# Optimization experiments

Measured on AMD Instinct MI355X. Metric: run time of the kernel, lower is better.

Reference implementation:

```python
import jax, jax.numpy as jnp
import numpy as np

B, T, I = 8192, 20, 16
H1, H2, FC = 128, 64, 32


def _lstm(x_tbi, Wih, Whh, bih, bhh, H):
    """PyTorch-convention LSTM. x_tbi: (T,B,in). Gate order: i,f,g,o. Returns (T,B,H) hidden seq."""
    Tn, Bn = x_tbi.shape[0], x_tbi.shape[1]
    # precompute input projection for all timesteps: (T,B,4H)
    xz = jnp.einsum('tbi,gi->tbg', x_tbi, Wih) + (bih + bhh)

    def step(carry, xz_t):
        h, c = carry
        z = xz_t + h @ Whh.T  # (B,4H)
        i = jax.nn.sigmoid(z[:, 0*H:1*H])
        f = jax.nn.sigmoid(z[:, 1*H:2*H])
        g = jnp.tanh(z[:, 2*H:3*H])
        o = jax.nn.sigmoid(z[:, 3*H:4*H])
        c = f * c + i * g
        h = o * jnp.tanh(c)
        return (h, c), h

    h0 = jnp.zeros((Bn, H), x_tbi.dtype)
    c0 = jnp.zeros((Bn, H), x_tbi.dtype)
    _, hs = jax.lax.scan(step, (h0, c0), xz)
    return hs  # (T,B,H)


def setup_inputs() -> dict:
    key = jax.random.key(0)
    ks = jax.random.split(key, 16)
    s1 = 1.0 / np.sqrt(H1)
    s2 = 1.0 / np.sqrt(H2)
    u = lambda k, shape, s: jax.random.uniform(k, shape, jnp.float32, -s, s)
    return {
        'x': jax.random.normal(ks[0], (B, T, I), jnp.float32),
        'Wih1': u(ks[1], (4 * H1, I), s1),
        'Whh1': u(ks[2], (4 * H1, H1), s1),
        'bih1': u(ks[3], (4 * H1,), s1),
        'bhh1': u(ks[4], (4 * H1,), s1),
        'Wih2': u(ks[5], (4 * H2, H1), s2),
        'Whh2': u(ks[6], (4 * H2, H2), s2),
        'bih2': u(ks[7], (4 * H2,), s2),
        'bhh2': u(ks[8], (4 * H2,), s2),
        'gamma': jnp.ones((H2,), jnp.float32),
        'beta': jnp.zeros((H2,), jnp.float32),
        'W1': u(ks[9], (FC, H2), 1.0 / np.sqrt(H2)),
        'b1': u(ks[10], (FC,), 1.0 / np.sqrt(H2)),
        'W2': u(ks[11], (1, FC), 1.0 / np.sqrt(FC)),
        'b2': u(ks[12], (1,), 1.0 / np.sqrt(FC)),
    }


def reference(x, Wih1, Whh1, bih1, bhh1, Wih2, Whh2, bih2, bhh2, gamma, beta, W1, b1, W2, b2):
    # dropout layers are identity (eval mode)
    x_tbi = jnp.transpose(x, (1, 0, 2))           # (T,B,I)
    out1 = _lstm(x_tbi, Wih1, Whh1, bih1, bhh1, H1)  # (T,B,H1)
    out2 = _lstm(out1, Wih2, Whh2, bih2, bhh2, H2)   # (T,B,H2)
    last = out2[-1]                               # (B,H2)
    # LayerNorm over H2
    mu = jnp.mean(last, axis=-1, keepdims=True)
    var = jnp.mean((last - mu) ** 2, axis=-1, keepdims=True)
    normed = (last - mu) * jax.lax.rsqrt(var + 1e-5) * gamma + beta
    h = jax.nn.relu(normed @ W1.T + b1)           # (B,FC)
    logit = h @ W2.T + b2                         # (B,1)
    return logit[:, 0]
```

## Files before the change

kernel.cpp:

```cpp
#include <hip/hip_runtime.h>

#define TS 20
#define BATCH 8192
#define LOG2E 1.4426950408889634f

typedef _Float16 half8 __attribute__((ext_vector_type(8)));
typedef float f32x4 __attribute__((ext_vector_type(4)));

__device__ __forceinline__ float fexp2(float x) {
#if __has_builtin(__builtin_amdgcn_exp2f)
    return __builtin_amdgcn_exp2f(x);
#else
    return exp2f(x);
#endif
}
__device__ __forceinline__ float sig2(float zp)  { return __builtin_amdgcn_rcpf(1.0f + fexp2(-zp)); }
__device__ __forceinline__ float tanh2(float zp) { return 1.0f - 2.0f * __builtin_amdgcn_rcpf(1.0f + fexp2(zp)); }
__device__ __forceinline__ int swz(int r) { return (r & 7) ^ (((r >> 3) & 1) << 2); }

extern "C" __global__ __launch_bounds__(512, 1)
void fused_lstm_kernel(const float* __restrict__ x,
                       const float* __restrict__ Wih1, const float* __restrict__ Whh1,
                       const float* __restrict__ bih1, const float* __restrict__ bhh1,
                       const float* __restrict__ Wih2, const float* __restrict__ Whh2,
                       const float* __restrict__ bih2, const float* __restrict__ bhh2,
                       const float* __restrict__ gamma, const float* __restrict__ beta,
                       const float* __restrict__ W1fc, const float* __restrict__ b1fc,
                       const float* __restrict__ W2fc, const float* __restrict__ b2fc,
                       float* __restrict__ out)
{
    __shared__ __align__(16) _Float16 bf2l[4 * 4 * 6 * 64 * 8];
    __shared__ __align__(16) _Float16 Hb[2][2][16][128];
    __shared__ __align__(16) _Float16 Hc[2][2][16][72];
    __shared__ __align__(16) _Float16 Xb[32][328];
    __shared__ float h2f[32][68];

    const int tid  = threadIdx.x;
    const int lane = tid & 63;
    const int w    = tid >> 6;
    const int lrow = lane & 15;
    const int lgrp = lane >> 4;
    const int b0   = blockIdx.x * 32;

    half8 bf[4][5];
    float bias1[4];
#pragma unroll
    for (int g = 0; g < 4; ++g) {
        const float sc = (g == 2) ? 2.0f * LOG2E : LOG2E;
        const int n = g * 128 + w * 16 + lrow;
        bias1[g] = (bih1[n] + bhh1[n]) * sc;
#pragma unroll
        for (int ch = 0; ch < 5; ++ch) {
            half8 v;
            if (ch < 4) {
                const float4 p0 = *(const float4*)&Whh1[n * 128 + ch * 32 + lgrp * 8];
                const float4 p1 = *(const float4*)&Whh1[n * 128 + ch * 32 + lgrp * 8 + 4];
                v[0]=(_Float16)(p0.x*sc); v[1]=(_Float16)(p0.y*sc); v[2]=(_Float16)(p0.z*sc); v[3]=(_Float16)(p0.w*sc);
                v[4]=(_Float16)(p1.x*sc); v[5]=(_Float16)(p1.y*sc); v[6]=(_Float16)(p1.z*sc); v[7]=(_Float16)(p1.w*sc);
            } else if (lgrp < 2) {
                const float4 p0 = *(const float4*)&Wih1[n * 16 + lgrp * 8];
                const float4 p1 = *(const float4*)&Wih1[n * 16 + lgrp * 8 + 4];
                v[0]=(_Float16)(p0.x*sc); v[1]=(_Float16)(p0.y*sc); v[2]=(_Float16)(p0.z*sc); v[3]=(_Float16)(p0.w*sc);
                v[4]=(_Float16)(p1.x*sc); v[5]=(_Float16)(p1.y*sc); v[6]=(_Float16)(p1.z*sc); v[7]=(_Float16)(p1.w*sc);
            } else {
#pragma unroll
                for (int j = 0; j < 8; ++j) v[j] = (_Float16)0.0f;
            }
            bf[g][ch] = v;
        }
    }

    const int cg = w & 3;
    const int mt = w >> 2;
    float bias2[4];
#pragma unroll
    for (int g = 0; g < 4; ++g) {
        const float sc = (g == 2) ? 2.0f * LOG2E : LOG2E;
        const int n = g * 64 + cg * 16 + lrow;
        bias2[g] = (bih2[n] + bhh2[n]) * sc;
    }
    if (w < 4) {
#pragma unroll
        for (int g = 0; g < 4; ++g) {
            const float sc = (g == 2) ? 2.0f * LOG2E : LOG2E;
            const int n = g * 64 + w * 16 + lrow;
#pragma unroll
            for (int ch = 0; ch < 6; ++ch) {
                const float4 p0 = (ch < 4) ? *(const float4*)&Wih2[n * 128 + ch * 32 + lgrp * 8]
                                           : *(const float4*)&Whh2[n * 64 + (ch - 4) * 32 + lgrp * 8];
                const float4 p1 = (ch < 4) ? *(const float4*)&Wih2[n * 128 + ch * 32 + lgrp * 8 + 4]
                                           : *(const float4*)&Whh2[n * 64 + (ch - 4) * 32 + lgrp * 8 + 4];
                half8 v;
                v[0]=(_Float16)(p0.x*sc); v[1]=(_Float16)(p0.y*sc); v[2]=(_Float16)(p0.z*sc); v[3]=(_Float16)(p0.w*sc);
                v[4]=(_Float16)(p1.x*sc); v[5]=(_Float16)(p1.y*sc); v[6]=(_Float16)(p1.z*sc); v[7]=(_Float16)(p1.w*sc);
                ((half8*)bf2l)[((w * 4 + g) * 6 + ch) * 64 + lane] = v;
            }
        }
    }

    for (int i = tid; i < 2 * 2 * 16 * 128; i += 512) (&Hb[0][0][0][0])[i] = (_Float16)0.0f;
    for (int i = tid; i < 2 * 2 * 16 * 72;  i += 512) (&Hc[0][0][0][0])[i] = (_Float16)0.0f;
    for (int i = tid; i < 32 * 320; i += 512) {
        const int r = i / 320, k = i % 320;
        Xb[r][k] = (_Float16)x[(size_t)(b0 + r) * 320 + k];
    }
    half8 kzero;
#pragma unroll
    for (int j = 0; j < 8; ++j) kzero[j] = (_Float16)0.0f;

    float c1[2][4] = {{0.f,0.f,0.f,0.f},{0.f,0.f,0.f,0.f}};
    float c2[4] = {0.f, 0.f, 0.f, 0.f};
    const int hu  = (w << 1) | (lrow >> 3);
    const int hlo = lrow & 7;
    const int szr = swz(lrow);
    const int cell2 = (cg << 4) | lrow;

    __syncthreads();

    for (int t = 0; t < TS; ++t) {
        const int s = t & 1;
        f32x4 z[2][4];
#pragma unroll
        for (int tile = 0; tile < 2; ++tile)
#pragma unroll
            for (int g = 0; g < 4; ++g) z[tile][g] = (f32x4){bias1[g], bias1[g], bias1[g], bias1[g]};
#pragma unroll
        for (int ch = 0; ch < 5; ++ch) {
#pragma unroll
            for (int tile = 0; tile < 2; ++tile) {
                half8 a;
                if (ch < 4) a = *(const half8*)&Hb[s ^ 1][tile][lrow][(((ch << 2) | lgrp) ^ szr) * 8];
                else        a = (lgrp < 2) ? *(const half8*)&Xb[tile * 16 + lrow][t * 16 + lgrp * 8] : kzero;
#pragma unroll
                for (int g = 0; g < 4; ++g)
                    z[tile][g] = __builtin_amdgcn_mfma_f32_16x16x32_f16(a, bf[g][ch], z[tile][g], 0, 0, 0);
            }
        }
#pragma unroll
        for (int tile = 0; tile < 2; ++tile)
#pragma unroll
            for (int j = 0; j < 4; ++j) {
                const float iv = sig2 (z[tile][0][j]);
                const float fv = sig2 (z[tile][1][j]);
                const float gv = tanh2(z[tile][2][j]);
                const float ov = sig2 (z[tile][3][j]);
                const float cn = fv * c1[tile][j] + iv * gv;
                c1[tile][j] = cn;
                const float h = ov * tanh2(2.0f * LOG2E * cn);
                const int m = (lgrp << 2) | j;
                Hb[s][tile][m][((hu ^ swz(m)) << 3) | hlo] = (_Float16)h;
            }
        __syncthreads();
        {
            half8 a2[6];
#pragma unroll
            for (int ch = 0; ch < 4; ++ch)
                a2[ch] = *(const half8*)&Hb[s][mt][lrow][(((ch << 2) | lgrp) ^ szr) * 8];
#pragma unroll
            for (int ch = 4; ch < 6; ++ch)
                a2[ch] = *(const half8*)&Hc[s ^ 1][mt][lrow][(ch - 4) * 32 + lgrp * 8];
            f32x4 z2[4];
#pragma unroll
            for (int g = 0; g < 4; ++g) {
                f32x4 acc = {bias2[g], bias2[g], bias2[g], bias2[g]};
#pragma unroll
                for (int ch = 0; ch < 6; ++ch) {
                    const half8 bfrag = ((const half8*)bf2l)[((cg * 4 + g) * 6 + ch) * 64 + lane];
                    acc = __builtin_amdgcn_mfma_f32_16x16x32_f16(a2[ch], bfrag, acc, 0, 0, 0);
                }
                z2[g] = acc;
            }
#pragma unroll
            for (int j = 0; j < 4; ++j) {
                const float iv = sig2 (z2[0][j]);
                const float fv = sig2 (z2[1][j]);
                const float gv = tanh2(z2[2][j]);
                const float ov = sig2 (z2[3][j]);
                const float cn = fv * c2[j] + iv * gv;
                c2[j] = cn;
                const float h = ov * tanh2(2.0f * LOG2E * cn);
                const int m = (lgrp << 2) | j;
                Hc[s][mt][m][cell2] = (_Float16)h;
                if (t == TS - 1) h2f[(mt << 4) | m][cell2] = h;
            }
        }
    }
    __syncthreads();

    {
        const int m = tid >> 4, q = tid & 15;
        const float v0 = h2f[m][q * 4 + 0];
        const float v1 = h2f[m][q * 4 + 1];
        const float v2 = h2f[m][q * 4 + 2];
        const float v3 = h2f[m][q * 4 + 3];
        float ssum = v0 + v1 + v2 + v3;
        ssum += __shfl_xor(ssum, 1); ssum += __shfl_xor(ssum, 2);
        ssum += __shfl_xor(ssum, 4); ssum += __shfl_xor(ssum, 8);
        const float mean = ssum * (1.0f / 64.0f);
        const float d0 = v0 - mean, d1 = v1 - mean, d2 = v2 - mean, d3 = v3 - mean;
        float vs = d0 * d0 + d1 * d1 + d2 * d2 + d3 * d3;
        vs += __shfl_xor(vs, 1); vs += __shfl_xor(vs, 2);
        vs += __shfl_xor(vs, 4); vs += __shfl_xor(vs, 8);
        const float rstd = rsqrtf(vs * (1.0f / 64.0f) + 1e-5f);
        const int i0 = q * 4;
        h2f[m][i0 + 0] = d0 * rstd * gamma[i0 + 0] + beta[i0 + 0];
        h2f[m][i0 + 1] = d1 * rstd * gamma[i0 + 1] + beta[i0 + 1];
        h2f[m][i0 + 2] = d2 * rstd * gamma[i0 + 2] + beta[i0 + 2];
        h2f[m][i0 + 3] = d3 * rstd * gamma[i0 + 3] + beta[i0 + 3];
    }
    __syncthreads();
    {
        const int o = tid & 31;
        const int mgrp = tid >> 5;
#pragma unroll
        for (int rr = 0; rr < 2; ++rr) {
            const int m = mgrp + rr * 16;
            float acc = b1fc[o];
#pragma unroll 8
            for (int k = 0; k < 64; ++k) acc += h2f[m][k] * W1fc[o * 64 + k];
            const float hv = fmaxf(acc, 0.0f);
            float p = hv * W2fc[o];
            p += __shfl_xor(p, 1); p += __shfl_xor(p, 2);
            p += __shfl_xor(p, 4); p += __shfl_xor(p, 8); p += __shfl_xor(p, 16);
            if (o == 0) out[b0 + m] = p + b2fc[0];
        }
    }
}

extern "C" void kernel_launch(void* const* d_in, const int* in_sizes, int n_in,
                              void* d_out, int out_size, void* d_ws, size_t ws_size,
                              hipStream_t stream) {
    (void)in_sizes; (void)n_in; (void)d_ws; (void)ws_size; (void)out_size;
    const float* x_p    = (const float*)d_in[0];
    const float* Wih1_p = (const float*)d_in[1];
    const float* Whh1_p = (const float*)d_in[2];
    const float* bih1_p = (const float*)d_in[3];
    const float* bhh1_p = (const float*)d_in[4];
    const float* Wih2_p = (const float*)d_in[5];
    const float* Whh2_p = (const float*)d_in[6];
    const float* bih2_p = (const float*)d_in[7];
    const float* bhh2_p = (const float*)d_in[8];
    const float* gamma_p = (const float*)d_in[9];
    const float* beta_p  = (const float*)d_in[10];
    const float* W1_p   = (const float*)d_in[11];
    const float* b1_p   = (const float*)d_in[12];
    const float* W2_p   = (const float*)d_in[13];
    const float* b2_p   = (const float*)d_in[14];
    float* out_p = (float*)d_out;

    fused_lstm_kernel<<<dim3(BATCH / 32), dim3(512), 0, stream>>>(
        x_p, Wih1_p, Whh1_p, bih1_p, bhh1_p,
        Wih2_p, Whh2_p, bih2_p, bhh2_p,
        gamma_p, beta_p, W1_p, b1_p, W2_p, b2_p, out_p);
}
```

Before: 77.85 us.

## Split LSTM layers into producer/consumer warp groups with 1024-thread blocks

Doubles the block to 1024 threads: waves 0-7 run layer 1 and waves 8-15 run layer 2 plus the head, so layer 2 at step t overlaps layer 1 at step t+1, coordinated by matched raw s_barrier calls. Layer-2 Wih2 fragments now live in registers and only Whh2 stays in shared memory, cutting LDS reads per step. This relies on an exact match of barrier counts between the two branches and raises register pressure per wave.

```diff
diff --git a/kernel.cpp b/kernel.cpp
--- a/kernel.cpp
+++ b/kernel.cpp
@@ -17,19 +17,23 @@
 __device__ __forceinline__ float sig2(float zp)  { return __builtin_amdgcn_rcpf(1.0f + fexp2(-zp)); }
 __device__ __forceinline__ float tanh2(float zp) { return 1.0f - 2.0f * __builtin_amdgcn_rcpf(1.0f + fexp2(zp)); }
 __device__ __forceinline__ int swz(int r) { return (r & 7) ^ (((r >> 3) & 1) << 2); }
-
-extern "C" __global__ __launch_bounds__(512, 1)
-void fused_lstm_kernel(const float* __restrict__ x,
-                       const float* __restrict__ Wih1, const float* __restrict__ Whh1,
-                       const float* __restrict__ bih1, const float* __restrict__ bhh1,
-                       const float* __restrict__ Wih2, const float* __restrict__ Whh2,
-                       const float* __restrict__ bih2, const float* __restrict__ bhh2,
-                       const float* __restrict__ gamma, const float* __restrict__ beta,
-                       const float* __restrict__ W1fc, const float* __restrict__ b1fc,
-                       const float* __restrict__ W2fc, const float* __restrict__ b2fc,
-                       float* __restrict__ out)
+__device__ __forceinline__ void wg_barrier() {
+    asm volatile("s_waitcnt lgkmcnt(0)" ::: "memory");
+    __builtin_amdgcn_s_barrier();
+}
+
+extern "C" __global__ __launch_bounds__(1024, 4)
+void fused_lstm_pc_kernel(const float* __restrict__ x,
+                          const float* __restrict__ Wih1, const float* __restrict__ Whh1,
+                          const float* __restrict__ bih1, const float* __restrict__ bhh1,
+                          const float* __restrict__ Wih2, const float* __restrict__ Whh2,
+                          const float* __restrict__ bih2, const float* __restrict__ bhh2,
+                          const float* __restrict__ gamma, const float* __restrict__ beta,
+                          const float* __restrict__ W1fc, const float* __restrict__ b1fc,
+                          const float* __restrict__ W2fc, const float* __restrict__ b2fc,
+                          float* __restrict__ out)
 {
-    __shared__ __align__(16) _Float16 bf2l[4 * 4 * 6 * 64 * 8];
+    __shared__ __align__(16) _Float16 bf2l[4 * 4 * 2 * 64 * 8];
     __shared__ __align__(16) _Float16 Hb[2][2][16][128];
     __shared__ __align__(16) _Float16 Hc[2][2][16][72];
     __shared__ __align__(16) _Float16 Xb[32][328];
@@ -42,133 +46,151 @@
     const int lgrp = lane >> 4;
     const int b0   = blockIdx.x * 32;
 
-    half8 bf[4][5];
-    float bias1[4];
-#pragma unroll
-    for (int g = 0; g < 4; ++g) {
-        const float sc = (g == 2) ? 2.0f * LOG2E : LOG2E;
-        const int n = g * 128 + w * 16 + lrow;
-        bias1[g] = (bih1[n] + bhh1[n]) * sc;
-#pragma unroll
-        for (int ch = 0; ch < 5; ++ch) {
-            half8 v;
-            if (ch < 4) {
-                const float4 p0 = *(const float4*)&Whh1[n * 128 + ch * 32 + lgrp * 8];
-                const float4 p1 = *(const float4*)&Whh1[n * 128 + ch * 32 + lgrp * 8 + 4];
-                v[0]=(_Float16)(p0.x*sc); v[1]=(_Float16)(p0.y*sc); v[2]=(_Float16)(p0.z*sc); v[3]=(_Float16)(p0.w*sc);
-                v[4]=(_Float16)(p1.x*sc); v[5]=(_Float16)(p1.y*sc); v[6]=(_Float16)(p1.z*sc); v[7]=(_Float16)(p1.w*sc);
-            } else if (lgrp < 2) {
-                const float4 p0 = *(const float4*)&Wih1[n * 16 + lgrp * 8];
-                const float4 p1 = *(const float4*)&Wih1[n * 16 + lgrp * 8 + 4];
-                v[0]=(_Float16)(p0.x*sc); v[1]=(_Float16)(p0.y*sc); v[2]=(_Float16)(p0.z*sc); v[3]=(_Float16)(p0.w*sc);
-                v[4]=(_Float16)(p1.x*sc); v[5]=(_Float16)(p1.y*sc); v[6]=(_Float16)(p1.z*sc); v[7]=(_Float16)(p1.w*sc);
-            } else {
-#pragma unroll
-                for (int j = 0; j < 8; ++j) v[j] = (_Float16)0.0f;
-            }
-            bf[g][ch] = v;
-        }
+    for (int i = tid; i < 2 * 2 * 16 * 128; i += 1024) (&Hb[0][0][0][0])[i] = (_Float16)0.0f;
+    for (int i = tid; i < 2 * 2 * 16 * 72;  i += 1024) (&Hc[0][0][0][0])[i] = (_Float16)0.0f;
+    for (int i = tid; i < 32 * 320; i += 1024) {
+        const int r = i / 320, k = i % 320;
+        Xb[r][k] = (_Float16)x[(size_t)(b0 + r) * 320 + k];
     }
 
-    const int cg = w & 3;
-    const int mt = w >> 2;
-    float bias2[4];
-#pragma unroll
-    for (int g = 0; g < 4; ++g) {
-        const float sc = (g == 2) ? 2.0f * LOG2E : LOG2E;
-        const int n = g * 64 + cg * 16 + lrow;
-        bias2[g] = (bih2[n] + bhh2[n]) * sc;
-    }
-    if (w < 4) {
+    if (w < 8) {
+        half8 bf[4][5];
+        float bias1[4];
 #pragma unroll
         for (int g = 0; g < 4; ++g) {
             const float sc = (g == 2) ? 2.0f * LOG2E : LOG2E;
-            const int n = g * 64 + w * 16 + lrow;
-#pragma unroll
-            for (int ch = 0; ch < 6; ++ch) {
-                const float4 p0 = (ch < 4) ? *(const float4*)&Wih2[n * 128 + ch * 32 + lgrp * 8]
-                                           : *(const float4*)&Whh2[n * 64 + (ch - 4) * 32 + lgrp * 8];
-                const float4 p1 = (ch < 4) ? *(const float4*)&Wih2[n * 128 + ch * 32 + lgrp * 8 + 4]
-                                           : *(const float4*)&Whh2[n * 64 + (ch - 4) * 32 + lgrp * 8 + 4];
+            const int n = g * 128 + w * 16 + lrow;
+            bias1[g] = (bih1[n] + bhh1[n]) * sc;
+#pragma unroll
+            for (int ch = 0; ch < 5; ++ch) {
+                half8 v;
+                if (ch < 4) {
+                    const float4 p0 = *(const float4*)&Whh1[n * 128 + ch * 32 + lgrp * 8];
+                    const float4 p1 = *(const float4*)&Whh1[n * 128 + ch * 32 + lgrp * 8 + 4];
+                    v[0]=(_Float16)(p0.x*sc); v[1]=(_Float16)(p0.y*sc); v[2]=(_Float16)(p0.z*sc); v[3]=(_Float16)(p0.w*sc);
+                    v[4]=(_Float16)(p1.x*sc); v[5]=(_Float16)(p1.y*sc); v[6]=(_Float16)(p1.z*sc); v[7]=(_Float16)(p1.w*sc);
+                } else if (lgrp < 2) {
+                    const float4 p0 = *(const float4*)&Wih1[n * 16 + lgrp * 8];
+                    const float4 p1 = *(const float4*)&Wih1[n * 16 + lgrp * 8 + 4];
+                    v[0]=(_Float16)(p0.x*sc); v[1]=(_Float16)(p0.y*sc); v[2]=(_Float16)(p0.z*sc); v[3]=(_Float16)(p0.w*sc);
+                    v[4]=(_Float16)(p1.x*sc); v[5]=(_Float16)(p1.y*sc); v[6]=(_Float16)(p1.z*sc); v[7]=(_Float16)(p1.w*sc);
+                } else {
+#pragma unroll
+                    for (int j = 0; j < 8; ++j) v[j] = (_Float16)0.0f;
+                }
+                bf[g][ch] = v;
+            }
+        }
+        half8 kzero;
+#pragma unroll
+        for (int j = 0; j < 8; ++j) kzero[j] = (_Float16)0.0f;
+
+        float c1[2][4] = {{0.f,0.f,0.f,0.f},{0.f,0.f,0.f,0.f}};
+        const int hu  = (w << 1) | (lrow >> 3);
+        const int hlo = lrow & 7;
+        const int szr = swz(lrow);
+
+        wg_barrier();
+        for (int t = 0; t < TS; ++t) {
+            const int s = t & 1;
+            f32x4 z[2][4];
+#pragma unroll
+            for (int tile = 0; tile < 2; ++tile)
+#pragma unroll
+                for (int g = 0; g < 4; ++g) z[tile][g] = (f32x4){bias1[g], bias1[g], bias1[g], bias1[g]};
+#pragma unroll
+            for (int ch = 0; ch < 5; ++ch) {
+#pragma unroll
+                for (int tile = 0; tile < 2; ++tile) {
+                    half8 a;
+                    if (ch < 4) a = *(const half8*)&Hb[s ^ 1][tile][lrow][(((ch << 2) | lgrp) ^ szr) * 8];
+                    else        a = (lgrp < 2) ? *(const half8*)&Xb[tile * 16 + lrow][t * 16 + lgrp * 8] : kzero;
+#pragma unroll
+                    for (int g = 0; g < 4; ++g)
+                        z[tile][g] = __builtin_amdgcn_mfma_f32_16x16x32_f16(a, bf[g][ch], z[tile][g], 0, 0, 0);
+                }
+            }
+#pragma unroll
+            for (int tile = 0; tile < 2; ++tile)
+#pragma unroll
+                for (int j = 0; j < 4; ++j) {
+                    const float iv = sig2 (z[tile][0][j]);
+                    const float fv = sig2 (z[tile][1][j]);
+                    const float gv = tanh2(z[tile][2][j]);
+                    const float ov = sig2 (z[tile][3][j]);
+                    const float cn = fv * c1[tile][j] + iv * gv;
+                    c1[tile][j] = cn;
+                    const float h = ov * tanh2(2.0f * LOG2E * cn);
+                    const int m = (lgrp << 2) | j;
+                    Hb[s][tile][m][((hu ^ swz(m)) << 3) | hlo] = (_Float16)h;
+                }
+            wg_barrier();
+        }
+        wg_barrier();
+        wg_barrier();
+    } else {
+        const int bw = w - 8;
+        const int cg = bw & 3;
+        const int mt = bw >> 2;
+        half8 w2[4][4];
+        float bias2[4];
+#pragma unroll
+        for (int g = 0; g < 4; ++g) {
+            const float sc = (g == 2) ? 2.0f * LOG2E : LOG2E;
+            const int n = g * 64 + cg * 16 + lrow;
+            bias2[g] = (bih2[n] + bhh2[n]) * sc;
+#pragma unroll
+            for (int ch = 0; ch < 4; ++ch) {
+                const float4 p0 = *(const float4*)&Wih2[n * 128 + ch * 32 + lgrp * 8];
+                const float4 p1 = *(const float4*)&Wih2[n * 128 + ch * 32 + lgrp * 8 + 4];
                 half8 v;
                 v[0]=(_Float16)(p0.x*sc); v[1]=(_Float16)(p0.y*sc); v[2]=(_Float16)(p0.z*sc); v[3]=(_Float16)(p0.w*sc);
                 v[4]=(_Float16)(p1.x*sc); v[5]=(_Float16)(p1.y*sc); v[6]=(_Float16)(p1.z*sc); v[7]=(_Float16)(p1.w*sc);
-                ((half8*)bf2l)[((w * 4 + g) * 6 + ch) * 64 + lane] = v;
-            }
-        }
-    }
-
-    for (int i = tid; i < 2 * 2 * 16 * 128; i += 512) (&Hb[0][0][0][0])[i] = (_Float16)0.0f;
-    for (int i = tid; i < 2 * 2 * 16 * 72;  i += 512) (&Hc[0][0][0][0])[i] = (_Float16)0.0f;
-    for (int i = tid; i < 32 * 320; i += 512) {
-        const int r = i / 320, k = i % 320;
-        Xb[r][k] = (_Float16)x[(size_t)(b0 + r) * 320 + k];
-    }
-    half8 kzero;
-#pragma unroll
-    for (int j = 0; j < 8; ++j) kzero[j] = (_Float16)0.0f;
-
-    float c1[2][4] = {{0.f,0.f,0.f,0.f},{0.f,0.f,0.f,0.f}};
-    float c2[4] = {0.f, 0.f, 0.f, 0.f};
-    const int hu  = (w << 1) | (lrow >> 3);
-    const int hlo = lrow & 7;
-    const int szr = swz(lrow);
-    const int cell2 = (cg << 4) | lrow;
-
-    __syncthreads();
-
-    for (int t = 0; t < TS; ++t) {
-        const int s = t & 1;
-        f32x4 z[2][4];
-#pragma unroll
-        for (int tile = 0; tile < 2; ++tile)
-#pragma unroll
-            for (int g = 0; g < 4; ++g) z[tile][g] = (f32x4){bias1[g], bias1[g], bias1[g], bias1[g]};
-#pragma unroll
-        for (int ch = 0; ch < 5; ++ch) {
-#pragma unroll
-            for (int tile = 0; tile < 2; ++tile) {
-                half8 a;
-                if (ch < 4) a = *(const half8*)&Hb[s ^ 1][tile][lrow][(((ch << 2) | lgrp) ^ szr) * 8];
-                else        a = (lgrp < 2) ? *(const half8*)&Xb[tile * 16 + lrow][t * 16 + lgrp * 8] : kzero;
+                w2[g][ch] = v;
+            }
+        }
+        if (bw < 4) {
+#pragma unroll
+            for (int g = 0; g < 4; ++g) {
+                const float sc = (g == 2) ? 2.0f * LOG2E : LOG2E;
+                const int n = g * 64 + bw * 16 + lrow;
+#pragma unroll
+                for (int c2i = 0; c2i < 2; ++c2i) {
+                    const float4 p0 = *(const float4*)&Whh2[n * 64 + c2i * 32 + lgrp * 8];
+                    const float4 p1 = *(const float4*)&Whh2[n * 64 + c2i * 32 + lgrp * 8 + 4];
+                    half8 v;
+                    v[0]=(_Float16)(p0.x*sc); v[1]=(_Float16)(p0.y*sc); v[2]=(_Float16)(p0.z*sc); v[3]=(_Float16)(p0.w*sc);
+                    v[4]=(_Float16)(p1.x*sc); v[5]=(_Float16)(p1.y*sc); v[6]=(_Float16)(p1.z*sc); v[7]=(_Float16)(p1.w*sc);
+                    ((half8*)bf2l)[((bw * 4 + g) * 2 + c2i) * 64 + lane] = v;
+                }
+            }
+        }
+        float c2[4] = {0.f, 0.f, 0.f, 0.f};
+        const int cell2 = (cg << 4) | lrow;
+        const int szr = swz(lrow);
+
+        wg_barrier();
+        for (int t = 0; t < TS; ++t) {
+            const int s = t & 1;
+            wg_barrier();
+            f32x4 z2[4];
+#pragma unroll
+            for (int g = 0; g < 4; ++g) z2[g] = (f32x4){bias2[g], bias2[g], bias2[g], bias2[g]};
+#pragma unroll
+            for (int ch = 0; ch < 4; ++ch) {
+                const half8 a2 = *(const half8*)&Hb[s][mt][lrow][(((ch << 2) | lgrp) ^ szr) * 8];
 #pragma unroll
                 for (int g = 0; g < 4; ++g)
-                    z[tile][g] = __builtin_amdgcn_mfma_f32_16x16x32_f16(a, bf[g][ch], z[tile][g], 0, 0, 0);
-            }
-        }
-#pragma unroll
-        for (int tile = 0; tile < 2; ++tile)
-#pragma unroll
-            for (int j = 0; j < 4; ++j) {
-                const float iv = sig2 (z[tile][0][j]);
-                const float fv = sig2 (z[tile][1][j]);
-                const float gv = tanh2(z[tile][2][j]);
-                const float ov = sig2 (z[tile][3][j]);
-                const float cn = fv * c1[tile][j] + iv * gv;
-                c1[tile][j] = cn;
-                const float h = ov * tanh2(2.0f * LOG2E * cn);
-                const int m = (lgrp << 2) | j;
-                Hb[s][tile][m][((hu ^ swz(m)) << 3) | hlo] = (_Float16)h;
-            }
-        __syncthreads();
-        {
-            half8 a2[6];
-#pragma unroll
-            for (int ch = 0; ch < 4; ++ch)
-                a2[ch] = *(const half8*)&Hb[s][mt][lrow][(((ch << 2) | lgrp) ^ szr) * 8];
-#pragma unroll
-            for (int ch = 4; ch < 6; ++ch)
-                a2[ch] = *(const half8*)&Hc[s ^ 1][mt][lrow][(ch - 4) * 32 + lgrp * 8];
-            f32x4 z2[4];
-#pragma unroll
-            for (int g = 0; g < 4; ++g) {
-                f32x4 acc = {bias2[g], bias2[g], bias2[g], bias2[g]};
-#pragma unroll
-                for (int ch = 0; ch < 6; ++ch) {
-                    const half8 bfrag = ((const half8*)bf2l)[((cg * 4 + g) * 6 + ch) * 64 + lane];
-                    acc = __builtin_amdgcn_mfma_f32_16x16x32_f16(a2[ch], bfrag, acc, 0, 0, 0);
-                }
-                z2[g] = acc;
+                    z2[g] = __builtin_amdgcn_mfma_f32_16x16x32_f16(a2, w2[g][ch], z2[g], 0, 0, 0);
+            }
+#pragma unroll
+            for (int c2i = 0; c2i < 2; ++c2i) {
+                const half8 a2 = *(const half8*)&Hc[s ^ 1][mt][lrow][c2i * 32 + lgrp * 8];
+#pragma unroll
+                for (int g = 0; g < 4; ++g) {
+                    const half8 bfrag = ((const half8*)bf2l)[((cg * 4 + g) * 2 + c2i) * 64 + lane];
+                    z2[g] = __builtin_amdgcn_mfma_f32_16x16x32_f16(a2, bfrag, z2[g], 0, 0, 0);
+                }
             }
 #pragma unroll
             for (int j = 0; j < 4; ++j) {
@@ -184,45 +206,46 @@
                 if (t == TS - 1) h2f[(mt << 4) | m][cell2] = h;
             }
         }
-    }
-    __syncthreads();
-
-    {
-        const int m = tid >> 4, q = tid & 15;
-        const float v0 = h2f[m][q * 4 + 0];
-        const float v1 = h2f[m][q * 4 + 1];
-        const float v2 = h2f[m][q * 4 + 2];
-        const float v3 = h2f[m][q * 4 + 3];
-        float ssum = v0 + v1 + v2 + v3;
-        ssum += __shfl_xor(ssum, 1); ssum += __shfl_xor(ssum, 2);
-        ssum += __shfl_xor(ssum, 4); ssum += __shfl_xor(ssum, 8);
-        const float mean = ssum * (1.0f / 64.0f);
-        const float d0 = v0 - mean, d1 = v1 - mean, d2 = v2 - mean, d3 = v3 - mean;
-        float vs = d0 * d0 + d1 * d1 + d2 * d2 + d3 * d3;
-        vs += __shfl_xor(vs, 1); vs += __shfl_xor(vs, 2);
-        vs += __shfl_xor(vs, 4); vs += __shfl_xor(vs, 8);
-        const float rstd = rsqrtf(vs * (1.0f / 64.0f) + 1e-5f);
-        const int i0 = q * 4;
-        h2f[m][i0 + 0] = d0 * rstd * gamma[i0 + 0] + beta[i0 + 0];
-        h2f[m][i0 + 1] = d1 * rstd * gamma[i0 + 1] + beta[i0 + 1];
-        h2f[m][i0 + 2] = d2 * rstd * gamma[i0 + 2] + beta[i0 + 2];
-        h2f[m][i0 + 3] = d3 * rstd * gamma[i0 + 3] + beta[i0 + 3];
-    }
-    __syncthreads();
-    {
-        const int o = tid & 31;
-        const int mgrp = tid >> 5;
-#pragma unroll
-        for (int rr = 0; rr < 2; ++rr) {
-            const int m = mgrp + rr * 16;
-            float acc = b1fc[o];
+        wg_barrier();
+        {
+            const int bt = tid - 512;
+            const int m = bt >> 4, q = bt & 15;
+            const float v0 = h2f[m][q * 4 + 0];
+            const float v1 = h2f[m][q * 4 + 1];
+            const float v2 = h2f[m][q * 4 + 2];
+            const float v3 = h2f[m][q * 4 + 3];
+            float ssum = v0 + v1 + v2 + v3;
+            ssum += __shfl_xor(ssum, 1); ssum += __shfl_xor(ssum, 2);
+            ssum += __shfl_xor(ssum, 4); ssum += __shfl_xor(ssum, 8);
+            const float mean = ssum * (1.0f / 64.0f);
+            const float d0 = v0 - mean, d1 = v1 - mean, d2 = v2 - mean, d3 = v3 - mean;
+            float vs = d0 * d0 + d1 * d1 + d2 * d2 + d3 * d3;
+            vs += __shfl_xor(vs, 1); vs += __shfl_xor(vs, 2);
+            vs += __shfl_xor(vs, 4); vs += __shfl_xor(vs, 8);
+            const float rstd = rsqrtf(vs * (1.0f / 64.0f) + 1e-5f);
+            const int i0 = q * 4;
+            h2f[m][i0 + 0] = d0 * rstd * gamma[i0 + 0] + beta[i0 + 0];
+            h2f[m][i0 + 1] = d1 * rstd * gamma[i0 + 1] + beta[i0 + 1];
+            h2f[m][i0 + 2] = d2 * rstd * gamma[i0 + 2] + beta[i0 + 2];
+            h2f[m][i0 + 3] = d3 * rstd * gamma[i0 + 3] + beta[i0 + 3];
+        }
+        wg_barrier();
+        {
+            const int bt = tid - 512;
+            const int o = bt & 31;
+            const int mgrp = bt >> 5;
+#pragma unroll
+            for (int rr = 0; rr < 2; ++rr) {
+                const int m = mgrp + rr * 16;
+                float acc = b1fc[o];
 #pragma unroll 8
-            for (int k = 0; k < 64; ++k) acc += h2f[m][k] * W1fc[o * 64 + k];
-            const float hv = fmaxf(acc, 0.0f);
-            float p = hv * W2fc[o];
-            p += __shfl_xor(p, 1); p += __shfl_xor(p, 2);
-            p += __shfl_xor(p, 4); p += __shfl_xor(p, 8); p += __shfl_xor(p, 16);
-            if (o == 0) out[b0 + m] = p + b2fc[0];
+                for (int k = 0; k < 64; ++k) acc += h2f[m][k] * W1fc[o * 64 + k];
+                const float hv = fmaxf(acc, 0.0f);
+                float p = hv * W2fc[o];
+                p += __shfl_xor(p, 1); p += __shfl_xor(p, 2);
+                p += __shfl_xor(p, 4); p += __shfl_xor(p, 8); p += __shfl_xor(p, 16);
+                if (o == 0) out[b0 + m] = p + b2fc[0];
+            }
         }
     }
 }
@@ -248,7 +271,7 @@
     const float* b2_p   = (const float*)d_in[14];
     float* out_p = (float*)d_out;
 
-    fused_lstm_kernel<<<dim3(BATCH / 32), dim3(512), 0, stream>>>(
+    fused_lstm_pc_kernel<<<dim3(BATCH / 32), dim3(1024), 0, stream>>>(
         x_p, Wih1_p, Whh1_p, bih1_p, bhh1_p,
         Wih2_p, Whh2_p, bih2_p, bhh2_p,
         gamma_p, beta_p, W1_p, b1_p, W2_p, b2_p, out_p);
```

New measurement: 127.0 us. 1.63x slower.

## Warp-specialize LSTM layers into pipelined producer and consumer wave groups

Applied to the files above, without the earlier changes.

Waves 0-3 now compute only layer 1 and each covers two gate column groups. Waves 4-7 compute only layer 2, running one timestep behind, so the two layers overlap instead of executing back to back each step. Layer-2 weights move from shared memory into registers, and the per-step barrier becomes a custom one that waits only on LDS traffic before `s_barrier`. The cost is twice the layer-1 MFMA work per producer wave on the critical path, plus higher register pressure.

```diff
diff --git a/kernel.cpp b/kernel.cpp
--- a/kernel.cpp
+++ b/kernel.cpp
@@ -17,19 +17,22 @@
 __device__ __forceinline__ float sig2(float zp)  { return __builtin_amdgcn_rcpf(1.0f + fexp2(-zp)); }
 __device__ __forceinline__ float tanh2(float zp) { return 1.0f - 2.0f * __builtin_amdgcn_rcpf(1.0f + fexp2(zp)); }
 __device__ __forceinline__ int swz(int r) { return (r & 7) ^ (((r >> 3) & 1) << 2); }
+__device__ __forceinline__ void wg_barrier() {
+    asm volatile("s_waitcnt lgkmcnt(0)" ::: "memory");
+    __builtin_amdgcn_s_barrier();
+}
 
 extern "C" __global__ __launch_bounds__(512, 1)
-void fused_lstm_kernel(const float* __restrict__ x,
-                       const float* __restrict__ Wih1, const float* __restrict__ Whh1,
-                       const float* __restrict__ bih1, const float* __restrict__ bhh1,
-                       const float* __restrict__ Wih2, const float* __restrict__ Whh2,
-                       const float* __restrict__ bih2, const float* __restrict__ bhh2,
-                       const float* __restrict__ gamma, const float* __restrict__ beta,
-                       const float* __restrict__ W1fc, const float* __restrict__ b1fc,
-                       const float* __restrict__ W2fc, const float* __restrict__ b2fc,
-                       float* __restrict__ out)
+void fused_lstm_pc8_kernel(const float* __restrict__ x,
+                           const float* __restrict__ Wih1, const float* __restrict__ Whh1,
+                           const float* __restrict__ bih1, const float* __restrict__ bhh1,
+                           const float* __restrict__ Wih2, const float* __restrict__ Whh2,
+                           const float* __restrict__ bih2, const float* __restrict__ bhh2,
+                           const float* __restrict__ gamma, const float* __restrict__ beta,
+                           const float* __restrict__ W1fc, const float* __restrict__ b1fc,
+                           const float* __restrict__ W2fc, const float* __restrict__ b2fc,
+                           float* __restrict__ out)
 {
-    __shared__ __align__(16) _Float16 bf2l[4 * 4 * 6 * 64 * 8];
     __shared__ __align__(16) _Float16 Hb[2][2][16][128];
     __shared__ __align__(16) _Float16 Hc[2][2][16][72];
     __shared__ __align__(16) _Float16 Xb[32][328];
@@ -42,48 +45,107 @@
     const int lgrp = lane >> 4;
     const int b0   = blockIdx.x * 32;
 
-    half8 bf[4][5];
-    float bias1[4];
-#pragma unroll
-    for (int g = 0; g < 4; ++g) {
-        const float sc = (g == 2) ? 2.0f * LOG2E : LOG2E;
-        const int n = g * 128 + w * 16 + lrow;
-        bias1[g] = (bih1[n] + bhh1[n]) * sc;
-#pragma unroll
-        for (int ch = 0; ch < 5; ++ch) {
-            half8 v;
-            if (ch < 4) {
-                const float4 p0 = *(const float4*)&Whh1[n * 128 + ch * 32 + lgrp * 8];
-                const float4 p1 = *(const float4*)&Whh1[n * 128 + ch * 32 + lgrp * 8 + 4];
-                v[0]=(_Float16)(p0.x*sc); v[1]=(_Float16)(p0.y*sc); v[2]=(_Float16)(p0.z*sc); v[3]=(_Float16)(p0.w*sc);
-                v[4]=(_Float16)(p1.x*sc); v[5]=(_Float16)(p1.y*sc); v[6]=(_Float16)(p1.z*sc); v[7]=(_Float16)(p1.w*sc);
-            } else if (lgrp < 2) {
-                const float4 p0 = *(const float4*)&Wih1[n * 16 + lgrp * 8];
-                const float4 p1 = *(const float4*)&Wih1[n * 16 + lgrp * 8 + 4];
-                v[0]=(_Float16)(p0.x*sc); v[1]=(_Float16)(p0.y*sc); v[2]=(_Float16)(p0.z*sc); v[3]=(_Float16)(p0.w*sc);
-                v[4]=(_Float16)(p1.x*sc); v[5]=(_Float16)(p1.y*sc); v[6]=(_Float16)(p1.z*sc); v[7]=(_Float16)(p1.w*sc);
-            } else {
-#pragma unroll
-                for (int j = 0; j < 8; ++j) v[j] = (_Float16)0.0f;
-            }
-            bf[g][ch] = v;
-        }
-    }
-
-    const int cg = w & 3;
-    const int mt = w >> 2;
-    float bias2[4];
-#pragma unroll
-    for (int g = 0; g < 4; ++g) {
-        const float sc = (g == 2) ? 2.0f * LOG2E : LOG2E;
-        const int n = g * 64 + cg * 16 + lrow;
-        bias2[g] = (bih2[n] + bhh2[n]) * sc;
-    }
+    for (int i = tid; i < 2 * 2 * 16 * 128; i += 512) (&Hb[0][0][0][0])[i] = (_Float16)0.0f;
+    for (int i = tid; i < 2 * 2 * 16 * 72;  i += 512) (&Hc[0][0][0][0])[i] = (_Float16)0.0f;
+    for (int i = tid; i < 32 * 320; i += 512) {
+        const int r = i / 320, k = i % 320;
+        Xb[r][k] = (_Float16)x[(size_t)(b0 + r) * 320 + k];
+    }
+
     if (w < 4) {
+        half8 bfw[2][4][5];
+        float bias1[2][4];
+#pragma unroll
+        for (int cgi = 0; cgi < 2; ++cgi) {
+            const int cg = w + cgi * 4;
+#pragma unroll
+            for (int g = 0; g < 4; ++g) {
+                const float sc = (g == 2) ? 2.0f * LOG2E : LOG2E;
+                const int n = g * 128 + cg * 16 + lrow;
+                bias1[cgi][g] = (bih1[n] + bhh1[n]) * sc;
+#pragma unroll
+                for (int ch = 0; ch < 5; ++ch) {
+                    half8 v;
+                    if (ch < 4) {
+                        const float4 p0 = *(const float4*)&Whh1[n * 128 + ch * 32 + lgrp * 8];
+                        const float4 p1 = *(const float4*)&Whh1[n * 128 + ch * 32 + lgrp * 8 + 4];
+                        v[0]=(_Float16)(p0.x*sc); v[1]=(_Float16)(p0.y*sc); v[2]=(_Float16)(p0.z*sc); v[3]=(_Float16)(p0.w*sc);
+                        v[4]=(_Float16)(p1.x*sc); v[5]=(_Float16)(p1.y*sc); v[6]=(_Float16)(p1.z*sc); v[7]=(_Float16)(p1.w*sc);
+                    } else if (lgrp < 2) {
+                        const float4 p0 = *(const float4*)&Wih1[n * 16 + lgrp * 8];
+                        const float4 p1 = *(const float4*)&Wih1[n * 16 + lgrp * 8 + 4];
+                        v[0]=(_Float16)(p0.x*sc); v[1]=(_Float16)(p0.y*sc); v[2]=(_Float16)(p0.z*sc); v[3]=(_Float16)(p0.w*sc);
+                        v[4]=(_Float16)(p1.x*sc); v[5]=(_Float16)(p1.y*sc); v[6]=(_Float16)(p1.z*sc); v[7]=(_Float16)(p1.w*sc);
+                    } else {
+#pragma unroll
+                        for (int j = 0; j < 8; ++j) v[j] = (_Float16)0.0f;
+                    }
+                    bfw[cgi][g][ch] = v;
+                }
+            }
+        }
+        half8 kzero;
+#pragma unroll
+        for (int j = 0; j < 8; ++j) kzero[j] = (_Float16)0.0f;
+
+        float c1[2][2][4] = {{{0.f,0.f,0.f,0.f},{0.f,0.f,0.f,0.f}},
+                             {{0.f,0.f,0.f,0.f},{0.f,0.f,0.f,0.f}}};
+        const int szr = swz(lrow);
+        const int hlo = lrow & 7;
+
+        wg_barrier();
+        for (int t = 0; t < TS; ++t) {
+            const int s = t & 1;
+#pragma unroll
+            for (int tile = 0; tile < 2; ++tile) {
+                half8 a[5];
+#pragma unroll
+                for (int ch = 0; ch < 4; ++ch)
+                    a[ch] = *(const half8*)&Hb[s ^ 1][tile][lrow][(((ch << 2) | lgrp) ^ szr) * 8];
+                a[4] = (lgrp < 2) ? *(const half8*)&Xb[tile * 16 + lrow][t * 16 + lgrp * 8] : kzero;
+
+                f32x4 z[2][4];
+#pragma unroll
+                for (int cgi = 0; cgi < 2; ++cgi)
+#pragma unroll
+                    for (int g = 0; g < 4; ++g)
+                        z[cgi][g] = (f32x4){bias1[cgi][g], bias1[cgi][g], bias1[cgi][g], bias1[cgi][g]};
+#pragma unroll
+                for (int ch = 0; ch < 5; ++ch)
+#pragma unroll
+                    for (int cgi = 0; cgi < 2; ++cgi)
+#pragma unroll
+                        for (int g = 0; g < 4; ++g)
+                            z[cgi][g] = __builtin_amdgcn_mfma_f32_16x16x32_f16(a[ch], bfw[cgi][g][ch], z[cgi][g], 0, 0, 0);
+#pragma unroll
+                for (int cgi = 0; cgi < 2; ++cgi) {
+                    const int cg = w + cgi * 4;
+                    const int hu = (cg << 1) | (lrow >> 3);
+#pragma unroll
+                    for (int j = 0; j < 4; ++j) {
+                        const float iv = sig2 (z[cgi][0][j]);
+                        const float fv = sig2 (z[cgi][1][j]);
+                        const float gv = tanh2(z[cgi][2][j]);
+                        const float ov = sig2 (z[cgi][3][j]);
+                        const float cn = fv * c1[tile][cgi][j] + iv * gv;
+                        c1[tile][cgi][j] = cn;
+                        const float h = ov * tanh2(2.0f * LOG2E * cn);
+                        const int m = (lgrp << 2) | j;
+                        Hb[s][tile][m][((hu ^ swz(m)) << 3) | hlo] = (_Float16)h;
+                    }
+                }
+            }
+            wg_barrier();
+        }
+    } else {
+        const int bw = w - 4;
+        half8 w2[4][6];
+        float bias2[4];
 #pragma unroll
         for (int g = 0; g < 4; ++g) {
             const float sc = (g == 2) ? 2.0f * LOG2E : LOG2E;
-            const int n = g * 64 + w * 16 + lrow;
+            const int n = g * 64 + bw * 16 + lrow;
+            bias2[g] = (bih2[n] + bhh2[n]) * sc;
 #pragma unroll
             for (int ch = 0; ch < 6; ++ch) {
                 const float4 p0 = (ch < 4) ? *(const float4*)&Wih2[n * 128 + ch * 32 + lgrp * 8]
@@ -93,95 +155,48 @@
                 half8 v;
                 v[0]=(_Float16)(p0.x*sc); v[1]=(_Float16)(p0.y*sc); v[2]=(_Float16)(p0.z*sc); v[3]=(_Float16)(p0.w*sc);
                 v[4]=(_Float16)(p1.x*sc); v[5]=(_Float16)(p1.y*sc); v[6]=(_Float16)(p1.z*sc); v[7]=(_Float16)(p1.w*sc);
-                ((half8*)bf2l)[((w * 4 + g) * 6 + ch) * 64 + lane] = v;
-            }
-        }
-    }
-
-    for (int i = tid; i < 2 * 2 * 16 * 128; i += 512) (&Hb[0][0][0][0])[i] = (_Float16)0.0f;
-    for (int i = tid; i < 2 * 2 * 16 * 72;  i += 512) (&Hc[0][0][0][0])[i] = (_Float16)0.0f;
-    for (int i = tid; i < 32 * 320; i += 512) {
-        const int r = i / 320, k = i % 320;
-        Xb[r][k] = (_Float16)x[(size_t)(b0 + r) * 320 + k];
-    }
-    half8 kzero;
-#pragma unroll
-    for (int j = 0; j < 8; ++j) kzero[j] = (_Float16)0.0f;
-
-    float c1[2][4] = {{0.f,0.f,0.f,0.f},{0.f,0.f,0.f,0.f}};
-    float c2[4] = {0.f, 0.f, 0.f, 0.f};
-    const int hu  = (w << 1) | (lrow >> 3);
-    const int hlo = lrow & 7;
-    const int szr = swz(lrow);
-    const int cell2 = (cg << 4) | lrow;
-
-    __syncthreads();
-
-    for (int t = 0; t < TS; ++t) {
-        const int s = t & 1;
-        f32x4 z[2][4];
-#pragma unroll
-        for (int tile = 0; tile < 2; ++tile)
-#pragma unroll
-            for (int g = 0; g < 4; ++g) z[tile][g] = (f32x4){bias1[g], bias1[g], bias1[g], bias1[g]};
-#pragma unroll
-        for (int ch = 0; ch < 5; ++ch) {
+                w2[g][ch] = v;
+            }
+        }
+        float c2[2][4] = {{0.f,0.f,0.f,0.f},{0.f,0.f,0.f,0.f}};
+        const int cell2 = (bw << 4) | lrow;
+        const int szr = swz(lrow);
+
+        wg_barrier();
+        for (int t = 0; t < TS; ++t) {
+            const int s = t & 1;
+            wg_barrier();
 #pragma unroll
             for (int tile = 0; tile < 2; ++tile) {
-                half8 a;
-                if (ch < 4) a = *(const half8*)&Hb[s ^ 1][tile][lrow][(((ch << 2) | lgrp) ^ szr) * 8];
-                else        a = (lgrp < 2) ? *(const half8*)&Xb[tile * 16 + lrow][t * 16 + lgrp * 8] : kzero;
+                half8 a2[6];
+#pragma unroll
+                for (int ch = 0; ch < 4; ++ch)
+                    a2[ch] = *(const half8*)&Hb[s][tile][lrow][(((ch << 2) | lgrp) ^ szr) * 8];
+#pragma unroll
+                for (int ch = 4; ch < 6; ++ch)
+                    a2[ch] = *(const half8*)&Hc[s ^ 1][tile][lrow][(ch - 4) * 32 + lgrp * 8];
+                f32x4 z2[4];
 #pragma unroll
                 for (int g = 0; g < 4; ++g)
-                    z[tile][g] = __builtin_amdgcn_mfma_f32_16x16x32_f16(a, bf[g][ch], z[tile][g], 0, 0, 0);
-            }
-        }
-#pragma unroll
-        for (int tile = 0; tile < 2; ++tile)
-#pragma unroll
-            for (int j = 0; j < 4; ++j) {
-                const float iv = sig2 (z[tile][0][j]);
-                const float fv = sig2 (z[tile][1][j]);
-                const float gv = tanh2(z[tile][2][j]);
-                const float ov = sig2 (z[tile][3][j]);
-                const float cn = fv * c1[tile][j] + iv * gv;
-                c1[tile][j] = cn;
-                const float h = ov * tanh2(2.0f * LOG2E * cn);
-                const int m = (lgrp << 2) | j;
-                Hb[s][tile][m][((hu ^ swz(m)) << 3) | hlo] = (_Float16)h;
-            }
-        __syncthreads();
-        {
-            half8 a2[6];
-#pragma unroll
-            for (int ch = 0; ch < 4; ++ch)
-                a2[ch] = *(const half8*)&Hb[s][mt][lrow][(((ch << 2) | lgrp) ^ szr) * 8];
-#pragma unroll
-            for (int ch = 4; ch < 6; ++ch)
-                a2[ch] = *(const half8*)&Hc[s ^ 1][mt][lrow][(ch - 4) * 32 + lgrp * 8];
-            f32x4 z2[4];
-#pragma unroll
-            for (int g = 0; g < 4; ++g) {
-                f32x4 acc = {bias2[g], bias2[g], bias2[g], bias2[g]};
-#pragma unroll
-                for (int ch = 0; ch < 6; ++ch) {
-                    const half8 bfrag = ((const half8*)bf2l)[((cg * 4 + g) * 6 + ch) * 64 + lane];
-                    acc = __builtin_amdgcn_mfma_f32_16x16x32_f16(a2[ch], bfrag, acc, 0, 0, 0);
+                    z2[g] = (f32x4){bias2[g], bias2[g], bias2[g], bias2[g]};
+#pragma unroll
+                for (int ch = 0; ch < 6; ++ch)
+#pragma unroll
+                    for (int g = 0; g < 4; ++g)
+                        z2[g] = __builtin_amdgcn_mfma_f32_16x16x32_f16(a2[ch], w2[g][ch], z2[g], 0, 0, 0);
+#pragma unroll
+                for (int j = 0; j < 4; ++j) {
+                    const float iv = sig2 (z2[0][j]);
+                    const float fv = sig2 (z2[1][j]);
+                    const float gv = tanh2(z2[2][j]);
+                    const float ov = sig2 (z2[3][j]);
+                    const float cn = fv * c2[tile][j] + iv * gv;
+                    c2[tile][j] = cn;
+                    const float h = ov * tanh2(2.0f * LOG2E * cn);
+                    const int m = (lgrp << 2) | j;
+                    Hc[s][tile][m][cell2] = (_Float16)h;
+                    if (t == TS - 1) h2f[(tile << 4) | m][cell2] = h;
                 }
-                z2[g] = acc;
-            }
-#pragma unroll
-            for (int j = 0; j < 4; ++j) {
-                const float iv = sig2 (z2[0][j]);
-                const float fv = sig2 (z2[1][j]);
-                const float gv = tanh2(z2[2][j]);
-                const float ov = sig2 (z2[3][j]);
-                const float cn = fv * c2[j] + iv * gv;
-                c2[j] = cn;
-                const float h = ov * tanh2(2.0f * LOG2E * cn);
-                const int m = (lgrp << 2) | j;
-                Hc[s][mt][m][cell2] = (_Float16)h;
-                if (t == TS - 1) h2f[(mt << 4) | m][cell2] = h;
             }
         }
     }
@@ -248,7 +263,7 @@
     const float* b2_p   = (const float*)d_in[14];
     float* out_p = (float*)d_out;
 
-    fused_lstm_kernel<<<dim3(BATCH / 32), dim3(512), 0, stream>>>(
+    fused_lstm_pc8_kernel<<<dim3(BATCH / 32), dim3(512), 0, stream>>>(
         x_p, Wih1_p, Whh1_p, bih1_p, bhh1_p,
         Wih2_p, Whh2_p, bih2_p, bhh2_p,
         gamma_p, beta_p, W1_p, b1_p, W2_p, b2_p, out_p);
```

After: 99.01 us. 1.27x slower.
